# Kernel tuning notes

Hardware: AMD Instinct MI355X
Metric: run time of the kernel (lower is better)

## Reference

```python
import jax, jax.numpy as jnp
import numpy as np

MAX_DISP = 4          # init kwarg
WIN = 2 * MAX_DISP + 1  # 9 -> 81 displacement offsets
CHUNK = 16            # hardcoded channel chunk size in the torch module


def setup_inputs() -> dict:
    key = jax.random.key(0)
    k1, k2 = jax.random.split(key)
    B, C, H, W = 8, 128, 96, 160
    x1 = jax.random.normal(k1, (B, C, H, W), dtype=jnp.float32)
    x2 = jax.random.normal(k2, (B, C, H, W), dtype=jnp.float32)
    return {"x1": x1, "x2": x2}


def reference(x1, x2):
    B, C, H, W = x2.shape
    pad = MAX_DISP
    # replicate padding == torch F.pad mode='replicate' == jnp 'edge'
    x2p = jnp.pad(x2, ((0, 0), (0, 0), (pad, pad), (pad, pad)), mode="edge")
    # offsets in the same row-major (dy outer, dx inner) order as the torch loops
    dy, dx = jnp.meshgrid(jnp.arange(-pad, pad + 1), jnp.arange(-pad, pad + 1), indexing="ij")
    offsets = jnp.stack([dy.ravel(), dx.ravel()], axis=1)  # [81, 2]
    num_chunks = -(-C // CHUNK)  # ceil(C/16); with C%16==0 chunk-mean == total-sum/num_chunks

    def body(carry, off):
        # shifted window of x2: x2p[:, :, pad+dy : pad+dy+H, pad+dx : pad+dx+W]
        sl = jax.lax.dynamic_slice(x2p, (0, 0, pad + off[0], pad + off[1]), (B, C, H, W))
        return carry, jnp.sum(x1 * sl, axis=1)  # [B, H, W]

    _, corr = jax.lax.scan(body, None, offsets)  # [81, B, H, W]
    corr = jnp.transpose(corr, (1, 0, 2, 3))     # [B, 81, H, W]
    return corr / jnp.asarray(num_chunks, corr.dtype)
```

## Files before the change

### kernel.cpp

```cpp
#include <hip/hip_runtime.h>
#include <cstdint>

#define BB 8
#define CC 128
#define HH 96
#define WW 160
#define HWsz (HH * WW)
#define TH 8
#define TW 32
#define CSTEP 8
#define HROWS 10
#define SW 48
#define CIW (HROWS * SW)
#define X2W (CSTEP * CIW)
#define X1W (CSTEP * TH * TW)
#define NWAVES 3
#define NTHREADS (NWAVES * 64)
#define NCHUNKS (CC / CSTEP)
#define NTILES (BB * (HH / TH) * (WW / TW))
#define NBLOCKS (NTILES * 3)
#define X1B (2 * X2W)

__device__ __forceinline__ void g2l_dword(const float* g, float* l) {
  __builtin_amdgcn_global_load_lds((const __attribute__((address_space(1))) void*)g,
                                   (__attribute__((address_space(3))) void*)l,
                                   4, 0, 0);
}

extern "C" __global__ void __launch_bounds__(NTHREADS, 2)
corr81_kernel(const float* __restrict__ x1, const float* __restrict__ x2,
              float* __restrict__ out)
{
  __shared__ __align__(16) float lds[2 * X2W + 2 * X1W];

  const int tid  = threadIdx.x;
  const int wvu  = __builtin_amdgcn_readfirstlane(tid >> 6);
  const int lane = tid & 63;
  const int h    = lane >> 5;
  const int r    = (lane >> 2) & 7;
  const int s    = lane & 3;

  const int bid0 = blockIdx.x;
  const int bid  = (bid0 & 7) * (NBLOCKS / 8) + (bid0 >> 3);
  const int tile = bid / 3;
  const int g    = bid - 3 * tile;
  const int wt   = tile % (WW / TW);
  const int ht   = (tile / (WW / TW)) % (HH / TH);
  const int b    = tile / ((WW / TW) * (HH / TH));
  const int h0   = ht * TH;
  const int w0   = wt * TW;
  const int hb   = h0 + 3 * g - 4;

  int grw[HROWS];
#pragma unroll
  for (int rr = 0; rr < HROWS; ++rr) {
    int v = hb + rr; v = v < 0 ? 0 : (v > HH - 1 ? HH - 1 : v);
    grw[rr] = v * WW;
  }
  int sc2[3], dc2[3], sx1[3], dx1[3];
#pragma unroll
  for (int c = 0; c < 3; ++c) {
    int ci = 3 * wvu + c; if (ci >= CSTEP) ci = 6;
    sc2[c] = ci * HWsz;
    dc2[c] = ci * CIW;
    sx1[c] = ci * HWsz;
    dx1[c] = ci * (TH * TW);
  }
  int hqw[4];
#pragma unroll
  for (int q = 0; q < 4; ++q) hqw[q] = (h0 + 2 * q) * WW + w0;

  int gw[4];
#pragma unroll
  for (int mm = 0; mm < 4; ++mm) {
    const int cl = lane ^ (mm << 2);
    int v = w0 + cl - 4;
    gw[mm] = v < 0 ? 0 : (v > WW - 1 ? WW - 1 : v);
  }
  {
  }
  const int hi1 = lane >> 5, lo1 = lane & 31;
  const int voffE = hi1 * WW + (lo1 ^ (hi1 << 2));
  const int voffO = hi1 * WW + (lo1 ^ ((2 | hi1) << 2));

  const float* x2b = x2 + (size_t)b * CC * HWsz;
  const float* x1b = x1 + (size_t)b * CC * HWsz;

  float acc[9][8];
#pragma unroll
  for (int d = 0; d < 9; ++d)
#pragma unroll
    for (int p = 0; p < 8; ++p) acc[d][p] = 0.f;

  const int R  = r + wvu;
  const int m2 = R & 3;
  int B4[4];
#pragma unroll
  for (int t = 0; t < 4; ++t)
    B4[t] = h * (4 * CIW) + R * SW + (((2 * s + t) ^ m2) << 2);
  const int m1 = r & 3;
  const int A0 = h * 1024 + r * TW + (((2 * s + 0) ^ m1) << 2);
  const int A1 = h * 1024 + r * TW + (((2 * s + 1) ^ m1) << 2);

#define STAGE(BUF, S2, S1)                                                   \
  {                                                                          \
    float* d2 = &lds[(BUF) * X2W];                                           \
    float* d1 = &lds[X1B + (BUF) * X1W];                                     \
    if (lane < SW) {                                                         \
      _Pragma("unroll")                                                      \
      for (int i = 0; i < 30; ++i) {                                         \
        const int c = i / 10, row = i % 10;                                  \
        g2l_dword((S2) + sc2[c] + grw[row] + gw[row & 3],                    \
                  d2 + dc2[c] + row * SW);                                   \
      }                                                                      \
    }                                                                        \
    _Pragma("unroll")                                                        \
    for (int i = 0; i < 12; ++i) {                                           \
      const int c = i / 4, q = i % 4;                                        \
      g2l_dword((S1) + sx1[c] + hqw[q] + ((q & 1) ? voffO : voffE),          \
                d1 + dx1[c] + q * 64);                                       \
    }                                                                        \
  }

#define COMPUTE(BUF)                                                         \
  {                                                                          \
    const float* xb = &lds[(BUF) * X2W];                                     \
    const float* ab = &lds[X1B + (BUF) * X1W];                               \
    _Pragma("unroll")                                                        \
    for (int q = 0; q < 4; ++q) {                           \
      const float4 a0 = *(const float4*)(ab + A0 + q * 256);                 \
      const float4 a1 = *(const float4*)(ab + A1 + q * 256);                 \
      const float av[8] = {a0.x, a0.y, a0.z, a0.w, a1.x, a1.y, a1.z, a1.w};  \
      float w16[16];                                                         \
      _Pragma("unroll")                                                      \
      for (int t = 0; t < 4; ++t) {                                          \
        const float4 f = *(const float4*)(xb + B4[t] + q * CIW);             \
        w16[4*t+0] = f.x; w16[4*t+1] = f.y;                                  \
        w16[4*t+2] = f.z; w16[4*t+3] = f.w;                                  \
      }                                                                      \
      _Pragma("unroll")                                                      \
      for (int d = 0; d < 9; ++d)                                            \
        _Pragma("unroll")                                                    \
        for (int p = 0; p < 8; ++p)                                          \
          acc[d][p] = fmaf(av[p], w16[d + p], acc[d][p]);                    \
    }                                                                        \
  }

  STAGE(0, x2b, x1b)

#pragma unroll 1
  for (int k = 0; k < NCHUNKS - 1; ++k) {
    {
      const float* s2 = x2b + (size_t)(k + 1) * (CSTEP * HWsz);
      const float* s1 = x1b + (size_t)(k + 1) * (CSTEP * HWsz);
      STAGE((k + 1) & 1, s2, s1)
    }

    __builtin_amdgcn_sched_barrier(0);
    asm volatile("s_waitcnt vmcnt(42)" ::: "memory");
    __builtin_amdgcn_sched_barrier(0);
    __builtin_amdgcn_s_barrier();
    __builtin_amdgcn_sched_barrier(0);

    COMPUTE(k & 1)

    __builtin_amdgcn_sched_barrier(0);
    __builtin_amdgcn_s_barrier();
    __builtin_amdgcn_sched_barrier(0);
  }

  asm volatile("s_waitcnt vmcnt(0)" ::: "memory");
  __builtin_amdgcn_sched_barrier(0);
  __builtin_amdgcn_s_barrier();
  __builtin_amdgcn_sched_barrier(0);
  COMPUTE((NCHUNKS - 1) & 1)

  const int dy = 3 * g + wvu;
  float* op = out + (((size_t)b * 81 + (size_t)dy * 9) * HH + (h0 + r)) * WW
                  + (w0 + 8 * s + 4 * h);
#pragma unroll
  for (int d = 0; d < 9; ++d) {
    const float own0 = h ? acc[d][4] : acc[d][0];
    const float own1 = h ? acc[d][5] : acc[d][1];
    const float own2 = h ? acc[d][6] : acc[d][2];
    const float own3 = h ? acc[d][7] : acc[d][3];
    const float snd0 = h ? acc[d][0] : acc[d][4];
    const float snd1 = h ? acc[d][1] : acc[d][5];
    const float snd2 = h ? acc[d][2] : acc[d][6];
    const float snd3 = h ? acc[d][3] : acc[d][7];
    float4 v;
    v.x = (own0 + __shfl_xor(snd0, 32)) * 0.125f;
    v.y = (own1 + __shfl_xor(snd1, 32)) * 0.125f;
    v.z = (own2 + __shfl_xor(snd2, 32)) * 0.125f;
    v.w = (own3 + __shfl_xor(snd3, 32)) * 0.125f;
    *(float4*)(op + (size_t)d * HWsz) = v;
  }
}

extern "C" void kernel_launch(void* const* d_in, const int* in_sizes, int n_in,
                              void* d_out, int out_size, void* d_ws, size_t ws_size,
                              hipStream_t stream) {
  const float* x1 = (const float*)d_in[0];
  const float* x2 = (const float*)d_in[1];
  float* out = (float*)d_out;
  corr81_kernel<<<dim3(NBLOCKS), dim3(NTHREADS), 0, stream>>>(x1, x2, out);
}
```

Before: 205.9 us.

## Stage tiles with 16-byte global-to-LDS loads plus border fixup

Global-to-LDS staging of x2 and x1 switches from per-dword to 16-byte global_load_lds. This cuts the issued load instructions per channel chunk from 42 to 8 and drops the lane<48 predication. The global addresses are permuted so the existing XOR-swizzled LDS layout is kept. Because 4-wide column blocks cannot express per-element replicate clamping at the left and right image edges, an in-LDS fixup pass rewrites the edge columns for border tiles before compute. The wait count is lowered to match the new instruction count.

```diff
diff --git a/kernel.cpp b/kernel.cpp
--- a/kernel.cpp
+++ b/kernel.cpp
@@ -21,10 +21,10 @@
 #define NBLOCKS (NTILES * 3)
 #define X1B (2 * X2W)
 
-__device__ __forceinline__ void g2l_dword(const float* g, float* l) {
+__device__ __forceinline__ void g2l_16(const float* g, float* l) {
   __builtin_amdgcn_global_load_lds((const __attribute__((address_space(1))) void*)g,
                                    (__attribute__((address_space(3))) void*)l,
-                                   4, 0, 0);
+                                   16, 0, 0);
 }
 
 extern "C" __global__ void __launch_bounds__(NTHREADS, 2)
@@ -51,37 +51,43 @@
   const int w0   = wt * TW;
   const int hb   = h0 + 3 * g - 4;
 
-  int grw[HROWS];
-#pragma unroll
-  for (int rr = 0; rr < HROWS; ++rr) {
-    int v = hb + rr; v = v < 0 ? 0 : (v > HH - 1 ? HH - 1 : v);
-    grw[rr] = v * WW;
-  }
-  int sc2[3], dc2[3], sx1[3], dx1[3];
-#pragma unroll
-  for (int c = 0; c < 3; ++c) {
-    int ci = 3 * wvu + c; if (ci >= CSTEP) ci = 6;
-    sc2[c] = ci * HWsz;
-    dc2[c] = ci * CIW;
-    sx1[c] = ci * HWsz;
-    dx1[c] = ci * (TH * TW);
-  }
-  int hqw[4];
-#pragma unroll
-  for (int q = 0; q < 4; ++q) hqw[q] = (h0 + 2 * q) * WW + w0;
-
-  int gw[4];
-#pragma unroll
-  for (int mm = 0; mm < 4; ++mm) {
-    const int cl = lane ^ (mm << 2);
-    int v = w0 + cl - 4;
-    gw[mm] = v < 0 ? 0 : (v > WW - 1 ? WW - 1 : v);
-  }
+  int soff2[5];
+#pragma unroll
+  for (int i = 0; i < 5; ++i) {
+    const int sl  = wvu + 3 * i;
+    const int w   = sl * 256 + 4 * lane;
+    const int ci  = w / CIW;
+    const int rem = w - ci * CIW;
+    const int row = rem / SW;
+    const int blk = (rem - row * SW) >> 2;
+    int gh = hb + row; gh = gh < 0 ? 0 : (gh > HH - 1 ? HH - 1 : gh);
+    int gc = w0 - 4 + 4 * (blk ^ (row & 3));
+    gc = gc < 0 ? 0 : (gc > WW - 4 ? WW - 4 : gc);
+    soff2[i] = ci * HWsz + gh * WW + gc;
+  }
+  const int xr  = lane >> 3;
+  const int xbk = lane & 7;
+  const int off1 = (h0 + xr) * WW + w0 + 4 * (xbk ^ (xr & 3));
+  int slx[3];
+#pragma unroll
+  for (int i = 0; i < 3; ++i) {
+    int sl = wvu + 3 * i; if (sl >= 8) sl = 5;
+    slx[i] = sl;
+  }
+
+  const bool doFix = (wt == 0) || (wt == (WW / TW - 1));
+  const int Lsrc = (wt == 0) ? 1 : 8;
+  const int wsrc = (wt == 0) ? 0 : 3;
+  const int Ldst = (wt == 0) ? 0 : 9;
+  int fixS1, fixD1, fixS2, fixD2;
   {
-  }
-  const int hi1 = lane >> 5, lo1 = lane & 31;
-  const int voffE = hi1 * WW + (lo1 ^ (hi1 << 2));
-  const int voffO = hi1 * WW + (lo1 ^ ((2 | hi1) << 2));
+    const int p1 = lane;      const int c1 = p1 / 10, r1 = p1 - 10 * c1;
+    fixS1 = c1 * CIW + r1 * SW + 4 * (Lsrc ^ (r1 & 3)) + wsrc;
+    fixD1 = c1 * CIW + r1 * SW + 4 * (Ldst ^ (r1 & 3));
+    const int p2 = 64 + lane; const int c2 = p2 / 10, r2 = p2 - 10 * c2;
+    fixS2 = c2 * CIW + r2 * SW + 4 * (Lsrc ^ (r2 & 3)) + wsrc;
+    fixD2 = c2 * CIW + r2 * SW + 4 * (Ldst ^ (r2 & 3));
+  }
 
   const float* x2b = x2 + (size_t)b * CC * HWsz;
   const float* x1b = x1 + (size_t)b * CC * HWsz;
@@ -105,27 +111,32 @@
 #define STAGE(BUF, S2, S1)                                                   \
   {                                                                          \
     float* d2 = &lds[(BUF) * X2W];                                           \
+    _Pragma("unroll")                                                        \
+    for (int i = 0; i < 5; ++i)                                              \
+      g2l_16((S2) + soff2[i], d2 + (wvu + 3 * i) * 256);                     \
     float* d1 = &lds[X1B + (BUF) * X1W];                                     \
-    if (lane < SW) {                                                         \
-      _Pragma("unroll")                                                      \
-      for (int i = 0; i < 30; ++i) {                                         \
-        const int c = i / 10, row = i % 10;                                  \
-        g2l_dword((S2) + sc2[c] + grw[row] + gw[row & 3],                    \
-                  d2 + dc2[c] + row * SW);                                   \
-      }                                                                      \
+    _Pragma("unroll")                                                        \
+    for (int i = 0; i < 3; ++i)                                              \
+      g2l_16((S1) + slx[i] * HWsz + off1, d1 + slx[i] * 256);                \
+  }
+
+#define FIXUP(CB)                                                            \
+  if (doFix) {                                                               \
+    float* fb = &lds[(CB) * X2W];                                            \
+    const float v1 = fb[fixS1];                                              \
+    float4 q1; q1.x = v1; q1.y = v1; q1.z = v1; q1.w = v1;                   \
+    *(float4*)(fb + fixD1) = q1;                                             \
+    if (lane < 16) {                                                         \
+      const float v2 = fb[fixS2];                                            \
+      float4 q2; q2.x = v2; q2.y = v2; q2.z = v2; q2.w = v2;                 \
+      *(float4*)(fb + fixD2) = q2;                                           \
     }                                                                        \
-    _Pragma("unroll")                                                        \
-    for (int i = 0; i < 12; ++i) {                                           \
-      const int c = i / 4, q = i % 4;                                        \
-      g2l_dword((S1) + sx1[c] + hqw[q] + ((q & 1) ? voffO : voffE),          \
-                d1 + dx1[c] + q * 64);                                       \
-    }                                                                        \
-  }
-
-#define COMPUTE(BUF)                                                         \
+  }
+
+#define COMPUTE(CB)                                                          \
   {                                                                          \
-    const float* xb = &lds[(BUF) * X2W];                                     \
-    const float* ab = &lds[X1B + (BUF) * X1W];                               \
+    const float* xb = &lds[(CB) * X2W];                                      \
+    const float* ab = &lds[X1B + (CB) * X1W];                                \
     _Pragma("unroll")                                                        \
     for (int q = 0; q < 4; ++q) {                           \
       const float4 a0 = *(const float4*)(ab + A0 + q * 256);                 \
@@ -157,9 +168,12 @@
     }
 
     __builtin_amdgcn_sched_barrier(0);
-    asm volatile("s_waitcnt vmcnt(42)" ::: "memory");
+    asm volatile("s_waitcnt vmcnt(8)" ::: "memory");
     __builtin_amdgcn_sched_barrier(0);
     __builtin_amdgcn_s_barrier();
+    __builtin_amdgcn_sched_barrier(0);
+
+    FIXUP(k & 1)
     __builtin_amdgcn_sched_barrier(0);
 
     COMPUTE(k & 1)
@@ -173,7 +187,9 @@
   __builtin_amdgcn_sched_barrier(0);
   __builtin_amdgcn_s_barrier();
   __builtin_amdgcn_sched_barrier(0);
-  COMPUTE((NCHUNKS - 1) & 1)
+  FIXUP(1)
+  __builtin_amdgcn_sched_barrier(0);
+  COMPUTE(1)
 
   const int dy = 3 * g + wvu;
   float* op = out + (((size_t)b * 81 + (size_t)dy * 9) * HH + (h0 + r)) * WW
```

Result: no change. 202.9 us (-1.4%).
